# Optimization experiments

Hardware: AMD Instinct MI355X
Metric: run time of the kernel (lower is better)

The kernel has to match this reference:

```python
import jax, jax.numpy as jnp
import numpy as np

SCALE = 1.0 / np.sqrt(128.0).astype(np.float32)  # 1/sqrt(head_dim)


def setup_inputs() -> dict:
    key = jax.random.key(0)
    kq, kk, kv = jax.random.split(key, 3)
    B, S, D = 32, 2048, 128
    q = jax.random.normal(kq, (B, S, D), dtype=jnp.float32)
    k = jax.random.normal(kk, (B, S, D), dtype=jnp.float32)
    v = jax.random.normal(kv, (B, S, D), dtype=jnp.float32)
    return {"q": q, "k": k, "v": v}


def reference(q, k, v):
    # attention = bmm(q, k^T) * scale ; softmax over last (key) dim; bmm with v
    scores = jnp.einsum("bsd,btd->bst", q, k) * SCALE  # [B, S, S]
    attn = jax.nn.softmax(scores, axis=-1)
    return jnp.einsum("bst,btd->bsd", attn, v)  # [B, S, D]
```

## Files before the change

kernel.cpp:

```cpp
#include <hip/hip_runtime.h>
#include <math.h>
#include <stdint.h>

typedef __bf16 bf16_t;
typedef __bf16 bf16x2 __attribute__((ext_vector_type(2)));
typedef __bf16 bf16x4 __attribute__((ext_vector_type(4)));
typedef __bf16 bf16x8 __attribute__((ext_vector_type(8)));
typedef float f32x4 __attribute__((ext_vector_type(4)));

#define NB   32
#define SEQ  2048
#define HD   128
#define SCALE 0.08838834764831845f

__global__ __launch_bounds__(256) void prep_kernel(
    const float* __restrict__ Q, const float* __restrict__ K,
    const float* __restrict__ V, bf16_t* __restrict__ Qs,
    bf16_t* __restrict__ Kb, bf16_t* __restrict__ Vt)
{
  const int b = blockIdx.x;
  const int tid = threadIdx.x;
  if (b < 4096) {
    const bool isQ = (b < 2048);
    const float* src = isQ ? Q : K;
    bf16_t* dst = isQ ? Qs : Kb;
    const float sc = isQ ? SCALE : 1.0f;
    size_t base4 = (size_t)(isQ ? b : b - 2048) * 1024;
#pragma unroll
    for (int i = 0; i < 4; ++i) {
      size_t idx = base4 + tid + i * 256;
      float4 x = ((const float4*)src)[idx];
      bf16x4 y;
      y[0] = (bf16_t)(x.x * sc); y[1] = (bf16_t)(x.y * sc);
      y[2] = (bf16_t)(x.z * sc); y[3] = (bf16_t)(x.w * sc);
      ((bf16x4*)dst)[idx] = y;
    }
  } else {
    __shared__ __attribute__((aligned(16))) bf16_t tile[64][72];
    const int bt = b - 4096;
    const int batch = bt >> 6;
    const int rem = bt & 63;
    const int s0 = (rem >> 1) * 64;
    const int d0 = (rem & 1) * 64;
#pragma unroll
    for (int i = 0; i < 4; ++i) {
      int e = tid + i * 256;
      int s = e >> 4, dq = e & 15;
      float4 x = *(const float4*)&V[((size_t)batch * SEQ + s0 + s) * HD + d0 + dq * 4];
      tile[dq * 4 + 0][s] = (bf16_t)x.x;
      tile[dq * 4 + 1][s] = (bf16_t)x.y;
      tile[dq * 4 + 2][s] = (bf16_t)x.z;
      tile[dq * 4 + 3][s] = (bf16_t)x.w;
    }
    __syncthreads();
#pragma unroll
    for (int i = 0; i < 2; ++i) {
      int g = tid + i * 256;
      int d = g >> 3, sg = g & 7;
      bf16x8 w = *(const bf16x8*)&tile[d][sg * 8];
      *(bf16x8*)&Vt[((size_t)batch * HD + d0 + d) * SEQ + s0 + sg * 8] = w;
    }
  }
}

__global__ __launch_bounds__(256) void fa5_kernel(
    const bf16_t* __restrict__ Qs, const bf16_t* __restrict__ Kbf,
    const bf16_t* __restrict__ Vt, float* __restrict__ O)
{
  __shared__ __attribute__((aligned(16))) bf16_t Ksw[2][64 * 128];
  __shared__ __attribute__((aligned(16))) bf16_t Vsw[2][128 * 64];
  __shared__ __attribute__((aligned(16))) bf16_t Psh[4][16][72];

  const int tid  = threadIdx.x;
  const int lane = tid & 63;
  const int wq   = tid >> 6;
  const int quad = lane >> 4;
  const int l15  = lane & 15;

  const int batch = blockIdx.x >> 5;
  const int qt    = blockIdx.x & 31;

  const bf16_t* Qb = Qs + ((size_t)batch * SEQ + qt * 64) * HD;
  const bf16_t* Kb = Kbf + (size_t)batch * SEQ * HD;
  const bf16_t* Vb = Vt + (size_t)batch * HD * SEQ;
  float*        Ob = O + ((size_t)batch * SEQ + qt * 64) * HD;

  bf16x8 aq[4];
  {
    const int qrow = wq * 16 + l15;
#pragma unroll
    for (int kf = 0; kf < 4; ++kf)
      aq[kf] = *(const bf16x8*)&Qb[(size_t)qrow * HD + kf * 32 + quad * 8];
  }

  f32x4 o[8];
#pragma unroll
  for (int t = 0; t < 8; ++t) { o[t][0]=0.f; o[t][1]=0.f; o[t][2]=0.f; o[t][3]=0.f; }
  float m_r = -INFINITY, l_r = 0.0f;

  auto stage = [&](int buf, int kb) {
#pragma unroll
    for (int i = 0; i < 4; ++i) {
      int row = wq * 16 + i * 4 + (lane >> 4);
      int gk = (lane & 15) ^ (row & 15);
      const bf16_t* gp = Kb + (size_t)(kb + row) * HD + gk * 8;
      __builtin_amdgcn_global_load_lds(
          (const __attribute__((address_space(1))) void*)gp,
          (__attribute__((address_space(3))) void*)&Ksw[buf][(wq * 16 + i * 4) * 128],
          16, 0, 0);
    }
#pragma unroll
    for (int i = 0; i < 4; ++i) {
      int d = wq * 32 + i * 8 + (lane >> 3);
      int gv = (lane & 7) ^ (d & 7);
      const bf16_t* gp = Vb + (size_t)d * SEQ + kb + gv * 8;
      __builtin_amdgcn_global_load_lds(
          (const __attribute__((address_space(1))) void*)gp,
          (__attribute__((address_space(3))) void*)&Vsw[buf][(wq * 32 + i * 8) * 64],
          16, 0, 0);
    }
  };

  stage(0, 0);

  for (int it = 0; it < SEQ / 64; ++it) {
    __syncthreads();
    if (it + 1 < SEQ / 64) stage((it + 1) & 1, (it + 1) * 64);

    const bf16_t* Ks = &Ksw[it & 1][0];
    const bf16_t* Vs = &Vsw[it & 1][0];

    f32x4 s[4];
#pragma unroll
    for (int ct = 0; ct < 4; ++ct) { s[ct][0]=0.f; s[ct][1]=0.f; s[ct][2]=0.f; s[ct][3]=0.f; }
#pragma unroll
    for (int kf = 0; kf < 4; ++kf)
#pragma unroll
      for (int ct = 0; ct < 4; ++ct) {
        int row = ct * 16 + l15;
        bf16x8 ak = *(const bf16x8*)&Ks[row * 128 + (((kf * 4 + quad) ^ l15) * 8)];
        s[ct] = __builtin_amdgcn_mfma_f32_16x16x32_bf16(ak, aq[kf], s[ct], 0, 0, 0);
      }

    float mx = s[0][0];
#pragma unroll
    for (int ct = 0; ct < 4; ++ct)
#pragma unroll
      for (int r = 0; r < 4; ++r) mx = fmaxf(mx, s[ct][r]);
    mx = fmaxf(mx, __shfl_xor(mx, 16));
    mx = fmaxf(mx, __shfl_xor(mx, 32));
    float mnew = fmaxf(m_r, mx);
    float alpha = __expf(m_r - mnew);
    m_r = mnew;
    float ls = 0.f;
#pragma unroll
    for (int ct = 0; ct < 4; ++ct)
#pragma unroll
      for (int r = 0; r < 4; ++r) {
        float p = __expf(s[ct][r] - mnew);
        s[ct][r] = p; ls += p;
      }
    ls += __shfl_xor(ls, 16);
    ls += __shfl_xor(ls, 32);
    l_r = l_r * alpha + ls;

#pragma unroll
    for (int ct = 0; ct < 4; ++ct) {
      bf16x4 pp;
      pp[0]=(bf16_t)s[ct][0]; pp[1]=(bf16_t)s[ct][1];
      pp[2]=(bf16_t)s[ct][2]; pp[3]=(bf16_t)s[ct][3];
      *(bf16x4*)&Psh[wq][l15][ct * 16 + quad * 4] = pp;
    }
    asm volatile("s_waitcnt lgkmcnt(0)" ::: "memory");
    bf16x8 ap0 = *(const bf16x8*)&Psh[wq][l15][quad * 8];
    bf16x8 ap1 = *(const bf16x8*)&Psh[wq][l15][32 + quad * 8];

#pragma unroll
    for (int t = 0; t < 8; ++t) {
      o[t][0]*=alpha; o[t][1]*=alpha; o[t][2]*=alpha; o[t][3]*=alpha;
    }
#pragma unroll
    for (int t = 0; t < 8; ++t) {
      int d = t * 16 + l15;
      bf16x8 av0 = *(const bf16x8*)&Vs[d * 64 + ((quad ^ (l15 & 7)) * 8)];
      o[t] = __builtin_amdgcn_mfma_f32_16x16x32_bf16(av0, ap0, o[t], 0, 0, 0);
      bf16x8 av1 = *(const bf16x8*)&Vs[d * 64 + (((4 + quad) ^ (l15 & 7)) * 8)];
      o[t] = __builtin_amdgcn_mfma_f32_16x16x32_bf16(av1, ap1, o[t], 0, 0, 0);
    }
  }

  float inv = 1.0f / l_r;
  const int qrow = wq * 16 + l15;
#pragma unroll
  for (int t = 0; t < 8; ++t) {
    float4 w;
    w.x = o[t][0]*inv; w.y = o[t][1]*inv; w.z = o[t][2]*inv; w.w = o[t][3]*inv;
    *(float4*)&Ob[(size_t)qrow * HD + t * 16 + quad * 4] = w;
  }
}

#define BM   64
#define BN   64
#define KPAD 8
#define VPAD 8
#define PPAD 8

__global__ __launch_bounds__(256) void fa_fallback(
    const float* __restrict__ Q, const float* __restrict__ K,
    const float* __restrict__ V, float* __restrict__ O)
{
  __shared__ __attribute__((aligned(16))) bf16_t Ksh[BN][HD + KPAD];
  __shared__ __attribute__((aligned(16))) bf16_t Vsh[HD][BN + VPAD];
  __shared__ __attribute__((aligned(16))) bf16_t Psh[4][16][BN + PPAD];

  const int tid = threadIdx.x;
  const int lane = tid & 63;
  const int wq = tid >> 6;
  const int quad = lane >> 4;
  const int l15 = lane & 15;
  const int bid = blockIdx.x;
  const int batch = bid >> 5;
  const int qt = bid & 31;

  const float* Qb = Q + (size_t)batch * SEQ * HD + (size_t)qt * BM * HD;
  const float* Kb = K + (size_t)batch * SEQ * HD;
  const float* Vb = V + (size_t)batch * SEQ * HD;
  float* Ob = O + (size_t)batch * SEQ * HD + (size_t)qt * BM * HD;

  bf16x8 aq[4];
  {
    const int qrow = wq * 16 + l15;
#pragma unroll
    for (int kf = 0; kf < 4; ++kf) {
      const float* qp = Qb + (size_t)qrow * HD + kf * 32 + quad * 8;
      float4 x0 = *(const float4*)(qp);
      float4 x1 = *(const float4*)(qp + 4);
      bf16x8 a;
      a[0] = (bf16_t)(x0.x * SCALE); a[1] = (bf16_t)(x0.y * SCALE);
      a[2] = (bf16_t)(x0.z * SCALE); a[3] = (bf16_t)(x0.w * SCALE);
      a[4] = (bf16_t)(x1.x * SCALE); a[5] = (bf16_t)(x1.y * SCALE);
      a[6] = (bf16_t)(x1.z * SCALE); a[7] = (bf16_t)(x1.w * SCALE);
      aq[kf] = a;
    }
  }

  f32x4 o[8];
#pragma unroll
  for (int t = 0; t < 8; ++t) { o[t][0]=0.f; o[t][1]=0.f; o[t][2]=0.f; o[t][3]=0.f; }
  float m_r = -INFINITY, l_r = 0.0f;
  const int vkp = (tid & 31) * 2;
  const int vg = tid >> 5;
  float4 kreg[8], vreg[8];

#pragma unroll
  for (int i = 0; i < 8; ++i) {
    int v = tid + i * 256, row = v >> 5, c4 = (v & 31) * 4;
    kreg[i] = *(const float4*)(Kb + (size_t)row * HD + c4);
  }
#pragma unroll
  for (int i = 0; i < 4; ++i) {
    int d0 = (vg + i * 8) * 4;
    const float* vp0 = Vb + (size_t)vkp * HD + d0;
    vreg[2 * i] = *(const float4*)vp0;
    vreg[2 * i + 1] = *(const float4*)(vp0 + HD);
  }

  for (int kb = 0; kb < SEQ; kb += BN) {
    __syncthreads();
#pragma unroll
    for (int i = 0; i < 8; ++i) {
      int v = tid + i * 256, row = v >> 5, c4 = (v & 31) * 4;
      float4 kv = kreg[i];
      bf16x4 kk;
      kk[0]=(bf16_t)kv.x; kk[1]=(bf16_t)kv.y; kk[2]=(bf16_t)kv.z; kk[3]=(bf16_t)kv.w;
      *(bf16x4*)&Ksh[row][c4] = kk;
    }
#pragma unroll
    for (int i = 0; i < 4; ++i) {
      int d0 = (vg + i * 8) * 4;
      float4 a0 = vreg[2 * i], a1 = vreg[2 * i + 1];
      bf16x2 p0; p0[0]=(bf16_t)a0.x; p0[1]=(bf16_t)a1.x;
      bf16x2 p1; p1[0]=(bf16_t)a0.y; p1[1]=(bf16_t)a1.y;
      bf16x2 p2; p2[0]=(bf16_t)a0.z; p2[1]=(bf16_t)a1.z;
      bf16x2 p3; p3[0]=(bf16_t)a0.w; p3[1]=(bf16_t)a1.w;
      *(bf16x2*)&Vsh[d0 + 0][vkp] = p0;
      *(bf16x2*)&Vsh[d0 + 1][vkp] = p1;
      *(bf16x2*)&Vsh[d0 + 2][vkp] = p2;
      *(bf16x2*)&Vsh[d0 + 3][vkp] = p3;
    }
    __syncthreads();

    const int kbn = kb + BN;
    if (kbn < SEQ) {
#pragma unroll
      for (int i = 0; i < 8; ++i) {
        int v = tid + i * 256, row = v >> 5, c4 = (v & 31) * 4;
        kreg[i] = *(const float4*)(Kb + (size_t)(kbn + row) * HD + c4);
      }
#pragma unroll
      for (int i = 0; i < 4; ++i) {
        int d0 = (vg + i * 8) * 4;
        const float* vp0 = Vb + (size_t)(kbn + vkp) * HD + d0;
        vreg[2 * i] = *(const float4*)vp0;
        vreg[2 * i + 1] = *(const float4*)(vp0 + HD);
      }
    }

    f32x4 s[4];
#pragma unroll
    for (int ct = 0; ct < 4; ++ct) { s[ct][0]=0.f; s[ct][1]=0.f; s[ct][2]=0.f; s[ct][3]=0.f; }
#pragma unroll
    for (int kf = 0; kf < 4; ++kf)
#pragma unroll
      for (int ct = 0; ct < 4; ++ct) {
        bf16x8 ak = *(const bf16x8*)&Ksh[ct * 16 + l15][kf * 32 + quad * 8];
        s[ct] = __builtin_amdgcn_mfma_f32_16x16x32_bf16(ak, aq[kf], s[ct], 0, 0, 0);
      }

    float mx = s[0][0];
#pragma unroll
    for (int ct = 0; ct < 4; ++ct)
#pragma unroll
      for (int r = 0; r < 4; ++r) mx = fmaxf(mx, s[ct][r]);
    mx = fmaxf(mx, __shfl_xor(mx, 16));
    mx = fmaxf(mx, __shfl_xor(mx, 32));
    float mnew = fmaxf(m_r, mx);
    float alpha = __expf(m_r - mnew);
    m_r = mnew;
    float ls = 0.f;
#pragma unroll
    for (int ct = 0; ct < 4; ++ct)
#pragma unroll
      for (int r = 0; r < 4; ++r) {
        float p = __expf(s[ct][r] - mnew);
        s[ct][r] = p; ls += p;
      }
    ls += __shfl_xor(ls, 16);
    ls += __shfl_xor(ls, 32);
    l_r = l_r * alpha + ls;

#pragma unroll
    for (int ct = 0; ct < 4; ++ct) {
      bf16x4 pp;
      pp[0]=(bf16_t)s[ct][0]; pp[1]=(bf16_t)s[ct][1];
      pp[2]=(bf16_t)s[ct][2]; pp[3]=(bf16_t)s[ct][3];
      *(bf16x4*)&Psh[wq][l15][ct * 16 + quad * 4] = pp;
    }
    asm volatile("s_waitcnt lgkmcnt(0)" ::: "memory");
    bf16x8 ap0 = *(const bf16x8*)&Psh[wq][l15][quad * 8];
    bf16x8 ap1 = *(const bf16x8*)&Psh[wq][l15][32 + quad * 8];

#pragma unroll
    for (int t = 0; t < 8; ++t) {
      o[t][0]*=alpha; o[t][1]*=alpha; o[t][2]*=alpha; o[t][3]*=alpha;
    }
#pragma unroll
    for (int t = 0; t < 8; ++t) {
      bf16x8 av0 = *(const bf16x8*)&Vsh[t * 16 + l15][quad * 8];
      o[t] = __builtin_amdgcn_mfma_f32_16x16x32_bf16(av0, ap0, o[t], 0, 0, 0);
      bf16x8 av1 = *(const bf16x8*)&Vsh[t * 16 + l15][32 + quad * 8];
      o[t] = __builtin_amdgcn_mfma_f32_16x16x32_bf16(av1, ap1, o[t], 0, 0, 0);
    }
  }

  float inv = 1.0f / l_r;
  const int qrow = wq * 16 + l15;
#pragma unroll
  for (int t = 0; t < 8; ++t) {
    float4 w;
    w.x = o[t][0]*inv; w.y = o[t][1]*inv; w.z = o[t][2]*inv; w.w = o[t][3]*inv;
    *(float4*)&Ob[(size_t)qrow * HD + t * 16 + quad * 4] = w;
  }
}

extern "C" void kernel_launch(void* const* d_in, const int* in_sizes, int n_in,
                              void* d_out, int out_size, void* d_ws, size_t ws_size,
                              hipStream_t stream) {
  const float* q = (const float*)d_in[0];
  const float* k = (const float*)d_in[1];
  const float* v = (const float*)d_in[2];
  float* out = (float*)d_out;

  const size_t elems = (size_t)NB * SEQ * HD;
  const size_t need = elems * 2 * 3;

  if (ws_size >= need) {
    bf16_t* Qs = (bf16_t*)d_ws;
    bf16_t* Kb = Qs + elems;
    bf16_t* Vt = Kb + elems;
    prep_kernel<<<6144, 256, 0, stream>>>(q, k, v, Qs, Kb, Vt);
    fa5_kernel<<<NB * (SEQ / 64), 256, 0, stream>>>(Qs, Kb, Vt, out);
  } else {
    fa_fallback<<<NB * (SEQ / BM), 256, 0, stream>>>(q, k, v, out);
  }
}
```

Baseline: 250.4 us.

## Fuse Q conversion into attention kernel, add lazy rescale and exp2 softmax

Q is now converted to bf16 and scaled by scale*log2e inside the attention kernel, which drops the Q pass and its workspace from the prep kernel. Softmax uses exp2 with a lazy rescale that only updates the running max when some row grows by more than 8. V fragment loads are hoisted ahead of the softmax, the l reduction is deferred, and s_setprio is raised around the MFMA blocks. The V transpose tile is now fp32 with padding. The lazy threshold lets unnormalized values grow up to 2^8, a small precision risk.

New measurement: 246.7 us. No clear change (-1.5%).

```diff
diff --git a/kernel.cpp b/kernel.cpp
--- a/kernel.cpp
+++ b/kernel.cpp
@@ -12,32 +12,36 @@
 #define SEQ  2048
 #define HD   128
 #define SCALE 0.08838834764831845f
+#define LOG2E 1.4426950408889634f
+
+__device__ __forceinline__ float fast_exp2(float x) {
+#if __has_builtin(__builtin_amdgcn_exp2f)
+  return __builtin_amdgcn_exp2f(x);
+#else
+  return exp2f(x);
+#endif
+}
 
 __global__ __launch_bounds__(256) void prep_kernel(
-    const float* __restrict__ Q, const float* __restrict__ K,
-    const float* __restrict__ V, bf16_t* __restrict__ Qs,
+    const float* __restrict__ K, const float* __restrict__ V,
     bf16_t* __restrict__ Kb, bf16_t* __restrict__ Vt)
 {
   const int b = blockIdx.x;
   const int tid = threadIdx.x;
-  if (b < 4096) {
-    const bool isQ = (b < 2048);
-    const float* src = isQ ? Q : K;
-    bf16_t* dst = isQ ? Qs : Kb;
-    const float sc = isQ ? SCALE : 1.0f;
-    size_t base4 = (size_t)(isQ ? b : b - 2048) * 1024;
+  if (b < 2048) {
+    size_t base4 = (size_t)b * 1024;
 #pragma unroll
     for (int i = 0; i < 4; ++i) {
       size_t idx = base4 + tid + i * 256;
-      float4 x = ((const float4*)src)[idx];
+      float4 x = ((const float4*)K)[idx];
       bf16x4 y;
-      y[0] = (bf16_t)(x.x * sc); y[1] = (bf16_t)(x.y * sc);
-      y[2] = (bf16_t)(x.z * sc); y[3] = (bf16_t)(x.w * sc);
-      ((bf16x4*)dst)[idx] = y;
+      y[0] = (bf16_t)x.x; y[1] = (bf16_t)x.y;
+      y[2] = (bf16_t)x.z; y[3] = (bf16_t)x.w;
+      ((bf16x4*)Kb)[idx] = y;
     }
   } else {
-    __shared__ __attribute__((aligned(16))) bf16_t tile[64][72];
-    const int bt = b - 4096;
+    __shared__ float tile[64][65];
+    const int bt = b - 2048;
     const int batch = bt >> 6;
     const int rem = bt & 63;
     const int s0 = (rem >> 1) * 64;
@@ -47,24 +51,26 @@
       int e = tid + i * 256;
       int s = e >> 4, dq = e & 15;
       float4 x = *(const float4*)&V[((size_t)batch * SEQ + s0 + s) * HD + d0 + dq * 4];
-      tile[dq * 4 + 0][s] = (bf16_t)x.x;
-      tile[dq * 4 + 1][s] = (bf16_t)x.y;
-      tile[dq * 4 + 2][s] = (bf16_t)x.z;
-      tile[dq * 4 + 3][s] = (bf16_t)x.w;
+      tile[s][dq * 4 + 0] = x.x;
+      tile[s][dq * 4 + 1] = x.y;
+      tile[s][dq * 4 + 2] = x.z;
+      tile[s][dq * 4 + 3] = x.w;
     }
     __syncthreads();
 #pragma unroll
     for (int i = 0; i < 2; ++i) {
       int g = tid + i * 256;
       int d = g >> 3, sg = g & 7;
-      bf16x8 w = *(const bf16x8*)&tile[d][sg * 8];
+      bf16x8 w;
+#pragma unroll
+      for (int j = 0; j < 8; ++j) w[j] = (bf16_t)tile[sg * 8 + j][d];
       *(bf16x8*)&Vt[((size_t)batch * HD + d0 + d) * SEQ + s0 + sg * 8] = w;
     }
   }
 }
 
-__global__ __launch_bounds__(256) void fa5_kernel(
-    const bf16_t* __restrict__ Qs, const bf16_t* __restrict__ Kbf,
+__global__ __launch_bounds__(256) void fa6_kernel(
+    const float* __restrict__ Q, const bf16_t* __restrict__ Kbf,
     const bf16_t* __restrict__ Vt, float* __restrict__ O)
 {
   __shared__ __attribute__((aligned(16))) bf16_t Ksw[2][64 * 128];
@@ -80,17 +86,27 @@
   const int batch = blockIdx.x >> 5;
   const int qt    = blockIdx.x & 31;
 
-  const bf16_t* Qb = Qs + ((size_t)batch * SEQ + qt * 64) * HD;
+  const float*  Qb = Q   + ((size_t)batch * SEQ + qt * 64) * HD;
   const bf16_t* Kb = Kbf + (size_t)batch * SEQ * HD;
-  const bf16_t* Vb = Vt + (size_t)batch * HD * SEQ;
-  float*        Ob = O + ((size_t)batch * SEQ + qt * 64) * HD;
+  const bf16_t* Vb = Vt  + (size_t)batch * HD * SEQ;
+  float*        Ob = O   + ((size_t)batch * SEQ + qt * 64) * HD;
 
   bf16x8 aq[4];
   {
     const int qrow = wq * 16 + l15;
-#pragma unroll
-    for (int kf = 0; kf < 4; ++kf)
-      aq[kf] = *(const bf16x8*)&Qb[(size_t)qrow * HD + kf * 32 + quad * 8];
+    const float qs = SCALE * LOG2E;
+#pragma unroll
+    for (int kf = 0; kf < 4; ++kf) {
+      const float* qp = Qb + (size_t)qrow * HD + kf * 32 + quad * 8;
+      float4 x0 = *(const float4*)qp;
+      float4 x1 = *(const float4*)(qp + 4);
+      bf16x8 a;
+      a[0] = (bf16_t)(x0.x * qs); a[1] = (bf16_t)(x0.y * qs);
+      a[2] = (bf16_t)(x0.z * qs); a[3] = (bf16_t)(x0.w * qs);
+      a[4] = (bf16_t)(x1.x * qs); a[5] = (bf16_t)(x1.y * qs);
+      a[6] = (bf16_t)(x1.z * qs); a[7] = (bf16_t)(x1.w * qs);
+      aq[kf] = a;
+    }
   }
 
   f32x4 o[8];
@@ -133,6 +149,7 @@
     f32x4 s[4];
 #pragma unroll
     for (int ct = 0; ct < 4; ++ct) { s[ct][0]=0.f; s[ct][1]=0.f; s[ct][2]=0.f; s[ct][3]=0.f; }
+    __builtin_amdgcn_s_setprio(1);
 #pragma unroll
     for (int kf = 0; kf < 4; ++kf)
 #pragma unroll
@@ -141,6 +158,7 @@
         bf16x8 ak = *(const bf16x8*)&Ks[row * 128 + (((kf * 4 + quad) ^ l15) * 8)];
         s[ct] = __builtin_amdgcn_mfma_f32_16x16x32_bf16(ak, aq[kf], s[ct], 0, 0, 0);
       }
+    __builtin_amdgcn_s_setprio(0);
 
     float mx = s[0][0];
 #pragma unroll
@@ -149,20 +167,34 @@
       for (int r = 0; r < 4; ++r) mx = fmaxf(mx, s[ct][r]);
     mx = fmaxf(mx, __shfl_xor(mx, 16));
     mx = fmaxf(mx, __shfl_xor(mx, 32));
-    float mnew = fmaxf(m_r, mx);
-    float alpha = __expf(m_r - mnew);
-    m_r = mnew;
+
+    bf16x8 av0[8], av1[8];
+#pragma unroll
+    for (int t = 0; t < 8; ++t) {
+      const int d = t * 16 + l15;
+      av0[t] = *(const bf16x8*)&Vs[d * 64 + ((quad ^ (l15 & 7)) * 8)];
+      av1[t] = *(const bf16x8*)&Vs[d * 64 + (((4 + quad) ^ (l15 & 7)) * 8)];
+    }
+
+    if (!__all(mx <= m_r + 8.0f)) {
+      const float mnew = fmaxf(m_r, mx);
+      const float alpha = fast_exp2(m_r - mnew);
+      m_r = mnew;
+      l_r *= alpha;
+#pragma unroll
+      for (int t = 0; t < 8; ++t) {
+        o[t][0]*=alpha; o[t][1]*=alpha; o[t][2]*=alpha; o[t][3]*=alpha;
+      }
+    }
+
     float ls = 0.f;
 #pragma unroll
     for (int ct = 0; ct < 4; ++ct)
 #pragma unroll
       for (int r = 0; r < 4; ++r) {
-        float p = __expf(s[ct][r] - mnew);
+        float p = fast_exp2(s[ct][r] - m_r);
         s[ct][r] = p; ls += p;
       }
-    ls += __shfl_xor(ls, 16);
-    ls += __shfl_xor(ls, 32);
-    l_r = l_r * alpha + ls;
 
 #pragma unroll
     for (int ct = 0; ct < 4; ++ct) {
@@ -171,22 +203,20 @@
       pp[2]=(bf16_t)s[ct][2]; pp[3]=(bf16_t)s[ct][3];
       *(bf16x4*)&Psh[wq][l15][ct * 16 + quad * 4] = pp;
     }
+    ls += __shfl_xor(ls, 16);
+    ls += __shfl_xor(ls, 32);
+    l_r += ls;
     asm volatile("s_waitcnt lgkmcnt(0)" ::: "memory");
     bf16x8 ap0 = *(const bf16x8*)&Psh[wq][l15][quad * 8];
     bf16x8 ap1 = *(const bf16x8*)&Psh[wq][l15][32 + quad * 8];
 
+    __builtin_amdgcn_s_setprio(1);
 #pragma unroll
     for (int t = 0; t < 8; ++t) {
-      o[t][0]*=alpha; o[t][1]*=alpha; o[t][2]*=alpha; o[t][3]*=alpha;
-    }
-#pragma unroll
-    for (int t = 0; t < 8; ++t) {
-      int d = t * 16 + l15;
-      bf16x8 av0 = *(const bf16x8*)&Vs[d * 64 + ((quad ^ (l15 & 7)) * 8)];
-      o[t] = __builtin_amdgcn_mfma_f32_16x16x32_bf16(av0, ap0, o[t], 0, 0, 0);
-      bf16x8 av1 = *(const bf16x8*)&Vs[d * 64 + (((4 + quad) ^ (l15 & 7)) * 8)];
-      o[t] = __builtin_amdgcn_mfma_f32_16x16x32_bf16(av1, ap1, o[t], 0, 0, 0);
-    }
+      o[t] = __builtin_amdgcn_mfma_f32_16x16x32_bf16(av0[t], ap0, o[t], 0, 0, 0);
+      o[t] = __builtin_amdgcn_mfma_f32_16x16x32_bf16(av1[t], ap1, o[t], 0, 0, 0);
+    }
+    __builtin_amdgcn_s_setprio(0);
   }
 
   float inv = 1.0f / l_r;
@@ -382,14 +412,13 @@
   float* out = (float*)d_out;
 
   const size_t elems = (size_t)NB * SEQ * HD;
-  const size_t need = elems * 2 * 3;
+  const size_t need = elems * 2 * 2;
 
   if (ws_size >= need) {
-    bf16_t* Qs = (bf16_t*)d_ws;
-    bf16_t* Kb = Qs + elems;
+    bf16_t* Kb = (bf16_t*)d_ws;
     bf16_t* Vt = Kb + elems;
-    prep_kernel<<<6144, 256, 0, stream>>>(q, k, v, Qs, Kb, Vt);
-    fa5_kernel<<<NB * (SEQ / 64), 256, 0, stream>>>(Qs, Kb, Vt, out);
+    prep_kernel<<<4096, 256, 0, stream>>>(k, v, Kb, Vt);
+    fa6_kernel<<<NB * (SEQ / 64), 256, 0, stream>>>(q, Kb, Vt, out);
   } else {
     fa_fallback<<<NB * (SEQ / BM), 256, 0, stream>>>(q, k, v, out);
   }
```
